# Kernel tuning notes

Measured on AMD Instinct MI355X. Metric: run time of the kernel, lower is better.

The kernel has to match this reference:

```python
import jax, jax.numpy as jnp
import numpy as np

ALPHA = 0.2  # LeakyReLU negative slope
NEG = -9e15

def _gat_head(Wh, a1, a2, adj_mask):
    # Wh: [N,O], a1/a2: [O], adj_mask: [N,N] bool
    e = jax.nn.leaky_relu(jnp.einsum('no,o->n', Wh, a1)[:, None]
                          + jnp.einsum('no,o->n', Wh, a2)[None, :], ALPHA)
    att = jax.nn.softmax(jnp.where(adj_mask, e, NEG), axis=-1)
    return att @ Wh  # [N,O]

def setup_inputs() -> dict:
    key = jax.random.key(0)
    ks = jax.random.split(key, 6)
    N, F_IN, O, H, C = 4096, 512, 64, 8, 16
    x = jax.random.normal(ks[0], (N, F_IN), jnp.float32)
    adj = jax.random.randint(ks[1], (N, N), 0, 2, jnp.int32)
    W = jax.random.normal(ks[2], (H, F_IN, O), jnp.float32) * 0.05
    a = jax.random.normal(ks[3], (H, 2 * O), jnp.float32) * 0.05
    W_out = jax.random.normal(ks[4], (H * O, C), jnp.float32) * 0.05
    a_out = jax.random.normal(ks[5], (2 * C,), jnp.float32) * 0.05
    return {'x': x, 'adj': adj, 'W': W, 'a': a, 'W_out': W_out, 'a_out': a_out}

def reference(x, adj, W, a, W_out, a_out):
    N = x.shape[0]
    H, _, O = W.shape
    C = W_out.shape[1]
    mask = adj > 0  # [N,N]
    # multi-head attention layer (vmapped over heads)
    Wh = jnp.einsum('nf,hfo->hno', x, W)  # [H,N,O]
    a1, a2 = a[:, :O], a[:, O:]
    h_heads = jax.vmap(_gat_head, in_axes=(0, 0, 0, None))(Wh, a1, a2, mask)  # [H,N,O]
    h = jax.nn.elu(h_heads)  # concat=True -> elu per head
    h = jnp.transpose(h, (1, 0, 2)).reshape(N, H * O)  # concat heads
    # output attention layer (concat=False)
    Wh_o = h @ W_out  # [N,C]
    out = _gat_head(Wh_o, a_out[:C], a_out[C:], mask)  # [N,C]
    out = jax.nn.elu(out)
    return jax.nn.log_softmax(out, axis=1)
```

## Files before the change

### kernel.cpp

```cpp
#include <hip/hip_runtime.h>


typedef __attribute__((ext_vector_type(8))) short short8;
typedef __attribute__((ext_vector_type(4))) float f32x4;
typedef unsigned long long u64;
typedef unsigned short u16;
typedef unsigned int u32;

__device__ __forceinline__ u16 f2bf_rne(float f){
  u32 u = __float_as_uint(f);
  return (u16)((u + 0x7fffu + ((u >> 16) & 1u)) >> 16);
}
__device__ __forceinline__ void async16(void* lds, const void* g){
  __builtin_amdgcn_global_load_lds((const __attribute__((address_space(1))) u32*)g,
                                   (__attribute__((address_space(3))) u32*)lds, 16, 0, 0);
}
__device__ __forceinline__ void async4(void* lds, const void* g){
  __builtin_amdgcn_global_load_lds((const __attribute__((address_space(1))) u32*)g,
                                   (__attribute__((address_space(3))) u32*)lds, 4, 0, 0);
}

__global__ __launch_bounds__(256) void k_adj_pack(const int* __restrict__ adj,
                                                  u64* __restrict__ bits){
  int lane = threadIdx.x & 63;
  int w0 = blockIdx.x * 4 + (threadIdx.x >> 6);
  #pragma unroll
  for (int k = 0; k < 16; ++k){
    int wid = w0 + k * 16384;
    int i  = wid >> 6;
    int jg = wid & 63;
    int v = adj[(size_t)i * 4096 + (jg << 6) + lane];
    u64 m = __ballot(v != 0);
    if (lane == 0) bits[(size_t)i * 64 + jg] = m;
  }
}

__global__ __launch_bounds__(256) void k_pack_in(const float* __restrict__ x,
                                                 const float* __restrict__ W,
                                                 u16* __restrict__ xA,
                                                 u16* __restrict__ wB){
  if (blockIdx.x < 1024){
    int tid = blockIdx.x * 256 + threadIdx.x;
    int n = tid & 4095;
    int fg = tid >> 12;
    const float* src = x + (size_t)n * 512 + fg * 8;
    float4 v0 = ((const float4*)src)[0];
    float4 v1 = ((const float4*)src)[1];
    u32 pk[4];
    pk[0] = f2bf_rne(v0.x) | ((u32)f2bf_rne(v0.y) << 16);
    pk[1] = f2bf_rne(v0.z) | ((u32)f2bf_rne(v0.w) << 16);
    pk[2] = f2bf_rne(v1.x) | ((u32)f2bf_rne(v1.y) << 16);
    pk[3] = f2bf_rne(v1.z) | ((u32)f2bf_rne(v1.w) << 16);
    *(uint4*)(xA + ((size_t)fg * 4096 + n) * 8) = *(uint4*)pk;
  } else {
    int tid = (blockIdx.x - 1024) * 256 + threadIdx.x;
    int o  = tid & 63;
    int fg = (tid >> 6) & 63;
    int h  = tid >> 12;
    const float* src = W + ((size_t)h * 512 + fg * 8) * 64 + o;
    u32 pk[4];
    #pragma unroll
    for (int p = 0; p < 4; ++p){
      u16 lo = f2bf_rne(src[(2 * p) * 64]);
      u16 hi = f2bf_rne(src[(2 * p + 1) * 64]);
      pk[p] = lo | ((u32)hi << 16);
    }
    *(uint4*)(wB + (size_t)h * 32768 + ((size_t)fg * 64 + o) * 8) = *(uint4*)pk;
  }
}

__global__ __launch_bounds__(256) void k_gemm1(const u16* __restrict__ xA,
                                               const u16* __restrict__ wB,
                                               const float* __restrict__ av,
                                               u16* __restrict__ whB,
                                               float* __restrict__ e11, float* __restrict__ e102,
                                               float* __restrict__ e21, float* __restrict__ e202){
  __shared__ u16 tr[4096];
  int h    = blockIdx.y;
  int nblk = blockIdx.x;
  int lane = threadIdx.x & 63;
  int wid  = threadIdx.x >> 6;
  int row16 = lane & 15, grp = lane >> 4;
  int n0 = nblk * 64;
  int n0w = n0 + wid * 16;
  const u16* wBh = wB + (size_t)h * 32768;
  f32x4 acc[4] = {};
  #pragma unroll 4
  for (int ks = 0; ks < 16; ++ks){
    int fgb = ks * 4 + grp;
    short8 af = *(const short8*)(xA + ((size_t)fgb * 4096 + n0w + row16) * 8);
    #pragma unroll
    for (int nt = 0; nt < 4; ++nt){
      short8 bf = *(const short8*)(wBh + ((size_t)fgb * 64 + nt * 16 + row16) * 8);
      acc[nt] = __builtin_amdgcn_mfma_f32_16x16x32_bf16(af, bf, acc[nt], 0, 0, 0);
    }
  }
  float a1v[4], a2v[4];
  #pragma unroll
  for (int nt = 0; nt < 4; ++nt){
    a1v[nt] = av[h * 128 + nt * 16 + row16];
    a2v[nt] = av[h * 128 + 64 + nt * 16 + row16];
  }
  #pragma unroll
  for (int r = 0; r < 4; ++r){
    float p1 = acc[0][r] * a1v[0] + acc[1][r] * a1v[1] + acc[2][r] * a1v[2] + acc[3][r] * a1v[3];
    float p2 = acc[0][r] * a2v[0] + acc[1][r] * a2v[1] + acc[2][r] * a2v[2] + acc[3][r] * a2v[3];
    #pragma unroll
    for (int d = 1; d < 16; d <<= 1){ p1 += __shfl_xor(p1, d, 64); p2 += __shfl_xor(p2, d, 64); }
    if (row16 == 0){
      int idx = h * 4096 + n0w + grp * 4 + r;
      e11[idx]  = __expf(p1); e102[idx] = __expf(0.2f * p1);
      e21[idx]  = __expf(p2); e202[idx] = __expf(0.2f * p2);
    }
  }
  #pragma unroll
  for (int nt = 0; nt < 4; ++nt)
    #pragma unroll
    for (int r = 0; r < 4; ++r){
      int jl = wid * 16 + grp * 4 + r;
      int o  = nt * 16 + row16;
      tr[((jl >> 3) * 64 + o) * 8 + (jl & 7)] = f2bf_rne(acc[nt][r]);
    }
  __syncthreads();
  u16* dst = whB + (size_t)h * 262144 + (size_t)n0 * 64;
  #pragma unroll
  for (int q = 0; q < 2; ++q)
    *(uint4*)(dst + (threadIdx.x * 2 + q) * 8) = *(const uint4*)(tr + (threadIdx.x * 2 + q) * 8);
}

__global__ __launch_bounds__(256) void k_att1(const u16* __restrict__ whB,
                                              const u64* __restrict__ adjbits,
                                              const float* __restrict__ e11, const float* __restrict__ e102,
                                              const float* __restrict__ e21, const float* __restrict__ e202,
                                              u16* __restrict__ pnum, float* __restrict__ pden){
  __shared__ u16  smB[2][4096];
  __shared__ float smT[2][2][64];
  __shared__ u32  smLut[4];
  int h     = blockIdx.y;
  int iblk  = blockIdx.x;
  int split = blockIdx.z;
  int lane = threadIdx.x & 63;
  int wid  = threadIdx.x >> 6;
  int row16 = lane & 15, grp = lane >> 4;
  if (threadIdx.x < 4)
    smLut[threadIdx.x] = ((threadIdx.x & 1) ? 0xFFFFu : 0u) | ((threadIdx.x & 2) ? 0xFFFF0000u : 0u);
  int ibase = iblk * 128 + wid * 32;
  int i0 = ibase + row16, i1 = ibase + 16 + row16;
  int hoff = h * 4096;
  float f1a  = e11[hoff + i0],  f1b  = e11[hoff + i1];
  float f02a = e102[hoff + i0], f02b = e102[hoff + i1];
  const u16* whBh = whB + (size_t)h * 262144;
  int jbeg = split * 1024;

  short8 bden;
  #pragma unroll
  for (int t = 0; t < 8; ++t) bden[t] = (row16 == 0) ? (short)0x3F80 : (short)0;

  auto stage = [&](int b, int j0){
    const char* g = (const char*)whBh + (size_t)j0 * 128 + wid * 2048 + lane * 16;
    char* l = (char*)(&smB[b][0]) + wid * 2048;
    async16(l, g);
    async16(l + 1024, g + 1024);
    if (wid == 0)      async4(&smT[b][0][0], (const char*)(e21  + hoff + j0) + lane * 4);
    else if (wid == 1) async4(&smT[b][1][0], (const char*)(e202 + hoff + j0) + lane * 4);
  };

  f32x4 acc[2][4] = {};
  f32x4 accden[2] = {};
  stage(0, jbeg);
  for (int c = 0; c < 16; ++c){
    int b = c & 1;
    u64 mrow0 = adjbits[(size_t)i0 * 64 + ((jbeg + c * 64) >> 6)];
    u64 mrow1 = adjbits[(size_t)i1 * 64 + ((jbeg + c * 64) >> 6)];
    __syncthreads();
    if (c < 15) stage(b ^ 1, jbeg + (c + 1) * 64);
    #pragma unroll
    for (int ks = 0; ks < 2; ++ks){
      int kb = ks * 32 + grp * 8;
      float4 eA = *(const float4*)(&smT[b][0][kb]);
      float4 eB = *(const float4*)(&smT[b][0][kb + 4]);
      float4 gA = *(const float4*)(&smT[b][1][kb]);
      float4 gB = *(const float4*)(&smT[b][1][kb + 4]);
      float e1v[8] = {eA.x, eA.y, eA.z, eA.w, eB.x, eB.y, eB.z, eB.w};
      float e2v[8] = {gA.x, gA.y, gA.z, gA.w, gB.x, gB.y, gB.z, gB.w};
      const u16* bbase = &smB[b][(ks * 4 + grp) * 512];
      short8 bf0 = *(const short8*)(bbase + (0 * 16 + row16) * 8);
      short8 bf1 = *(const short8*)(bbase + (1 * 16 + row16) * 8);
      short8 bf2 = *(const short8*)(bbase + (2 * 16 + row16) * 8);
      short8 bf3 = *(const short8*)(bbase + (3 * 16 + row16) * 8);
      #pragma unroll
      for (int it = 0; it < 2; ++it){
        u64 mrow = it ? mrow1 : mrow0;
        float f1 = it ? f1b : f1a;
        float f02 = it ? f02b : f02a;
        u32 mb = ((u32)(mrow >> (ks * 32)) >> (grp * 8)) & 0xffu;
        u32 pk[4];
        #pragma unroll
        for (int t2 = 0; t2 < 4; ++t2){
          float w0 = fmaxf(f1 * e1v[2 * t2],     f02 * e2v[2 * t2]);
          float w1 = fmaxf(f1 * e1v[2 * t2 + 1], f02 * e2v[2 * t2 + 1]);
          u32 p = __builtin_amdgcn_perm(__float_as_uint(w1), __float_as_uint(w0), 0x07060302u);
          pk[t2] = p & smLut[(mb >> (2 * t2)) & 3u];
        }
        short8 af = *(short8*)pk;
        acc[it][0] = __builtin_amdgcn_mfma_f32_16x16x32_bf16(af, bf0, acc[it][0], 0, 0, 0);
        acc[it][1] = __builtin_amdgcn_mfma_f32_16x16x32_bf16(af, bf1, acc[it][1], 0, 0, 0);
        acc[it][2] = __builtin_amdgcn_mfma_f32_16x16x32_bf16(af, bf2, acc[it][2], 0, 0, 0);
        acc[it][3] = __builtin_amdgcn_mfma_f32_16x16x32_bf16(af, bf3, acc[it][3], 0, 0, 0);
        accden[it] = __builtin_amdgcn_mfma_f32_16x16x32_bf16(af, bden, accden[it], 0, 0, 0);
      }
    }
  }

  #pragma unroll
  for (int it = 0; it < 2; ++it){
    #pragma unroll
    for (int r = 0; r < 4; ++r){
      int n = ibase + it * 16 + grp * 4 + r;
      if (row16 == 0)
        pden[((size_t)split * 8 + h) * 4096 + n] = accden[it][r];
      u16* dst = pnum + ((size_t)split * 4096 + n) * 512 + h * 64 + row16;
      #pragma unroll
      for (int nt = 0; nt < 4; ++nt)
        dst[nt * 16] = f2bf_rne(acc[it][nt][r]);
    }
  }
}

__global__ __launch_bounds__(256) void k_gemm2(const u16* __restrict__ pnum,
                                               const float* __restrict__ pden,
                                               const float* __restrict__ Wout,
                                               const float* __restrict__ aout,
                                               u16* __restrict__ whoB,
                                               float* __restrict__ e11o, float* __restrict__ e102o,
                                               float* __restrict__ e21o, float* __restrict__ e202o){
  __shared__ float Wl[8192];
  __shared__ float hrow[16 * 516];
  __shared__ float sden[128];
  int n0 = blockIdx.x * 16;
  for (int t = threadIdx.x; t < 8192; t += 256) Wl[t] = Wout[t];
  if (threadIdx.x < 128){
    int hh = threadIdx.x >> 4, nn = threadIdx.x & 15;
    float d = 0.f;
    #pragma unroll
    for (int s = 0; s < 4; ++s) d += pden[((size_t)s * 8 + hh) * 4096 + n0 + nn];
    sden[threadIdx.x] = d;
  }
  __syncthreads();
  {
    int nn = threadIdx.x >> 4;
    int fc = threadIdx.x & 15;
    int f0 = fc * 32;
    int hh = fc >> 1;
    float dinv = 1.f / sden[hh * 16 + nn];
    float v[32];
    #pragma unroll
    for (int k = 0; k < 32; ++k) v[k] = 0.f;
    #pragma unroll
    for (int s = 0; s < 4; ++s){
      const u16* p = pnum + ((size_t)s * 4096 + n0 + nn) * 512 + f0;
      #pragma unroll
      for (int q = 0; q < 4; ++q){
        uint4 raw = *(const uint4*)(p + q * 8);
        u32 rw[4] = {raw.x, raw.y, raw.z, raw.w};
        #pragma unroll
        for (int d2 = 0; d2 < 4; ++d2){
          v[q * 8 + d2 * 2]     += __uint_as_float(rw[d2] << 16);
          v[q * 8 + d2 * 2 + 1] += __uint_as_float(rw[d2] & 0xffff0000u);
        }
      }
    }
    #pragma unroll
    for (int k = 0; k < 32; ++k){
      float val = v[k] * dinv;
      val = val > 0.f ? val : (__expf(val) - 1.f);
      hrow[nn * 516 + f0 + k] = val;
    }
  }
  __syncthreads();
  int c  = threadIdx.x & 15;
  int rl = threadIdx.x >> 4;
  int n = n0 + rl;
  const float4* hr = (const float4*)(hrow + rl * 516);
  float acc = 0.f;
  #pragma unroll 8
  for (int f4 = 0; f4 < 128; ++f4){
    float4 hv = hr[f4];
    int f = f4 * 4;
    acc += hv.x * Wl[f * 16 + c] + hv.y * Wl[(f + 1) * 16 + c]
         + hv.z * Wl[(f + 2) * 16 + c] + hv.w * Wl[(f + 3) * 16 + c];
  }
  whoB[((size_t)(n >> 3) * 16 + c) * 8 + (n & 7)] = f2bf_rne(acc);
  float p1 = acc * aout[c], p2 = acc * aout[16 + c];
  #pragma unroll
  for (int d = 1; d < 16; d <<= 1){ p1 += __shfl_xor(p1, d, 64); p2 += __shfl_xor(p2, d, 64); }
  if (c == 0){
    e11o[n] = __expf(p1); e102o[n] = __expf(0.2f * p1);
    e21o[n] = __expf(p2); e202o[n] = __expf(0.2f * p2);
  }
}

__global__ __launch_bounds__(256) void k_att2(const u16* __restrict__ whoB,
                                              const u64* __restrict__ adjbits,
                                              const float* __restrict__ e11o, const float* __restrict__ e102o,
                                              const float* __restrict__ e21o, const float* __restrict__ e202o,
                                              float* __restrict__ pnum, float* __restrict__ pden){
  __shared__ u16  smB[2][1024];
  __shared__ float smT[2][2][64];
  __shared__ u32  smLut[4];
  int iblk  = blockIdx.x;
  int split = blockIdx.y;
  int lane = threadIdx.x & 63;
  int wid  = threadIdx.x >> 6;
  int row16 = lane & 15, grp = lane >> 4;
  if (threadIdx.x < 4)
    smLut[threadIdx.x] = ((threadIdx.x & 1) ? 0xFFFFu : 0u) | ((threadIdx.x & 2) ? 0xFFFF0000u : 0u);
  int i = iblk * 64 + wid * 16 + row16;
  float f1  = e11o[i];
  float f02 = e102o[i];
  int jbeg = split * 256;
  short8 bden;
  #pragma unroll
  for (int t = 0; t < 8; ++t) bden[t] = (row16 == 0) ? (short)0x3F80 : (short)0;

  auto stage = [&](int b, int j0){
    const char* gB = (const char*)whoB + (size_t)j0 * 32;
    if (wid == 0){
      async16((char*)&smB[b][0], gB + lane * 16);
      async16((char*)&smB[b][0] + 1024, gB + 1024 + lane * 16);
    }
    else if (wid == 1) async4(&smT[b][0][0], (const char*)(e21o  + j0) + lane * 4);
    else if (wid == 2) async4(&smT[b][1][0], (const char*)(e202o + j0) + lane * 4);
  };

  f32x4 acc = {};
  f32x4 accden = {};
  stage(0, jbeg);
  for (int c = 0; c < 4; ++c){
    int b = c & 1;
    u64 mrow = adjbits[(size_t)i * 64 + ((jbeg + c * 64) >> 6)];
    __syncthreads();
    if (c < 3) stage(b ^ 1, jbeg + (c + 1) * 64);
    #pragma unroll
    for (int ks = 0; ks < 2; ++ks){
      int kb = ks * 32 + grp * 8;
      float4 eA = *(const float4*)(&smT[b][0][kb]);
      float4 eB = *(const float4*)(&smT[b][0][kb + 4]);
      float4 gA = *(const float4*)(&smT[b][1][kb]);
      float4 gB = *(const float4*)(&smT[b][1][kb + 4]);
      float e1v[8] = {eA.x, eA.y, eA.z, eA.w, eB.x, eB.y, eB.z, eB.w};
      float e2v[8] = {gA.x, gA.y, gA.z, gA.w, gB.x, gB.y, gB.z, gB.w};
      u32 mb = ((u32)(mrow >> (ks * 32)) >> (grp * 8)) & 0xffu;
      u32 pk[4];
      #pragma unroll
      for (int t2 = 0; t2 < 4; ++t2){
        float w0 = fmaxf(f1 * e1v[2 * t2],     f02 * e2v[2 * t2]);
        float w1 = fmaxf(f1 * e1v[2 * t2 + 1], f02 * e2v[2 * t2 + 1]);
        u32 p = __builtin_amdgcn_perm(__float_as_uint(w1), __float_as_uint(w0), 0x07060302u);
        pk[t2] = p & smLut[(mb >> (2 * t2)) & 3u];
      }
      short8 af = *(short8*)pk;
      short8 bf = *(const short8*)(&smB[b][((ks * 4 + grp) * 16 + row16) * 8]);
      acc    = __builtin_amdgcn_mfma_f32_16x16x32_bf16(af, bf, acc, 0, 0, 0);
      accden = __builtin_amdgcn_mfma_f32_16x16x32_bf16(af, bden, accden, 0, 0, 0);
    }
  }
  #pragma unroll
  for (int r = 0; r < 4; ++r){
    int n = iblk * 64 + wid * 16 + grp * 4 + r;
    if (row16 == 0)
      pden[(size_t)n * 16 + split] = accden[r];
    pnum[((size_t)n * 16 + split) * 16 + row16] = acc[r];
  }
}

__global__ __launch_bounds__(256) void k_final(const float* __restrict__ pnum,
                                               const float* __restrict__ pden,
                                               float* __restrict__ out){
  int tid = blockIdx.x * 256 + threadIdx.x;
  int c = tid & 15;
  int n = tid >> 4;
  float num = 0.f, den = 0.f;
  #pragma unroll
  for (int s = 0; s < 16; ++s){
    num += pnum[((size_t)n * 16 + s) * 16 + c];
    den += pden[(size_t)n * 16 + s];
  }
  float v = num / den;
  v = v > 0.f ? v : (__expf(v) - 1.f);
  float m = v;
  #pragma unroll
  for (int d = 1; d < 16; d <<= 1) m = fmaxf(m, __shfl_xor(m, d, 64));
  float es = __expf(v - m), ss = es;
  #pragma unroll
  for (int d = 1; d < 16; d <<= 1) ss += __shfl_xor(ss, d, 64);
  out[(size_t)n * 16 + c] = v - m - __logf(ss);
}

extern "C" void kernel_launch(void* const* d_in, const int* in_sizes, int n_in,
                              void* d_out, int out_size, void* d_ws, size_t ws_size,
                              hipStream_t stream){
  (void)in_sizes; (void)n_in; (void)out_size; (void)ws_size;
  const float* x    = (const float*)d_in[0];
  const int*   adj  = (const int*)d_in[1];
  const float* W    = (const float*)d_in[2];
  const float* av   = (const float*)d_in[3];
  const float* Wout = (const float*)d_in[4];
  const float* aout = (const float*)d_in[5];
  float* out = (float*)d_out;
  char* ws = (char*)d_ws;

  u64*  adjbits = (u64*)(ws + 0x0000000);
  u16*  whB     = (u16*)(ws + 0x0200000);
  float* e11    = (float*)(ws + 0x0600000);
  float* e102   = (float*)(ws + 0x0620000);
  float* e21    = (float*)(ws + 0x0640000);
  float* e202   = (float*)(ws + 0x0660000);
  u16*  xA    = (u16*)(ws + 0x0680000);
  u16*  wB    = (u16*)(ws + 0x0A80000);
  u16*  pnum1 = (u16*)(ws + 0x0680000);
  float* pden1 = (float*)(ws + 0x1680000);
  u16*  whoB   = (u16*)(ws + 0x1700000);
  float* e11o  = (float*)(ws + 0x1720000);
  float* e102o = (float*)(ws + 0x1724000);
  float* e21o  = (float*)(ws + 0x1728000);
  float* e202o = (float*)(ws + 0x172C000);
  float* pnum2 = (float*)(ws + 0x1730000);
  float* pden2 = (float*)(ws + 0x1B30000);

  k_adj_pack<<<dim3(4096), dim3(256), 0, stream>>>(adj, adjbits);
  k_pack_in<<<dim3(1152), dim3(256), 0, stream>>>(x, W, xA, wB);
  k_gemm1<<<dim3(64, 8), dim3(256), 0, stream>>>(xA, wB, av, whB, e11, e102, e21, e202);
  k_att1<<<dim3(32, 8, 4), dim3(256), 0, stream>>>(whB, adjbits, e11, e102, e21, e202, pnum1, pden1);
  k_gemm2<<<dim3(256), dim3(256), 0, stream>>>(pnum1, pden1, Wout, aout, whoB, e11o, e102o, e21o, e202o);
  k_att2<<<dim3(64, 16), dim3(256), 0, stream>>>(whoB, adjbits, e11o, e102o, e21o, e202o, pnum2, pden2);
  k_final<<<dim3(256), dim3(256), 0, stream>>>(pnum2, pden2, out);
}
```

Baseline: 194.1 us.

## Load attention B-operands directly from global instead of LDS double-buffer staging

Both attention kernels drop the async global-to-LDS double-buffered staging of the value tiles and exp-score vectors. Each wave now reads its MFMA B fragments and score vectors straight from global memory, relying on L1/L2 caching, which removes the per-chunk block barriers and the LDS traffic. The cost is that the four waves re-fetch the same tiles redundantly through cache, with no explicit prefetch to hide load latency.

Measured after the change: 213.6 us. +10.1%, slower.

```diff
diff --git a/kernel.cpp b/kernel.cpp
--- a/kernel.cpp
+++ b/kernel.cpp
@@ -10,14 +10,6 @@
 __device__ __forceinline__ u16 f2bf_rne(float f){
   u32 u = __float_as_uint(f);
   return (u16)((u + 0x7fffu + ((u >> 16) & 1u)) >> 16);
-}
-__device__ __forceinline__ void async16(void* lds, const void* g){
-  __builtin_amdgcn_global_load_lds((const __attribute__((address_space(1))) u32*)g,
-                                   (__attribute__((address_space(3))) u32*)lds, 16, 0, 0);
-}
-__device__ __forceinline__ void async4(void* lds, const void* g){
-  __builtin_amdgcn_global_load_lds((const __attribute__((address_space(1))) u32*)g,
-                                   (__attribute__((address_space(3))) u32*)lds, 4, 0, 0);
 }
 
 __global__ __launch_bounds__(256) void k_adj_pack(const int* __restrict__ adj,
@@ -133,9 +125,7 @@
                                               const float* __restrict__ e11, const float* __restrict__ e102,
                                               const float* __restrict__ e21, const float* __restrict__ e202,
                                               u16* __restrict__ pnum, float* __restrict__ pden){
-  __shared__ u16  smB[2][4096];
-  __shared__ float smT[2][2][64];
-  __shared__ u32  smLut[4];
+  __shared__ u32 smLut[4];
   int h     = blockIdx.y;
   int iblk  = blockIdx.x;
   int split = blockIdx.z;
@@ -144,6 +134,7 @@
   int row16 = lane & 15, grp = lane >> 4;
   if (threadIdx.x < 4)
     smLut[threadIdx.x] = ((threadIdx.x & 1) ? 0xFFFFu : 0u) | ((threadIdx.x & 2) ? 0xFFFF0000u : 0u);
+  __syncthreads();
   int ibase = iblk * 128 + wid * 32;
   int i0 = ibase + row16, i1 = ibase + 16 + row16;
   int hoff = h * 4096;
@@ -156,38 +147,29 @@
   #pragma unroll
   for (int t = 0; t < 8; ++t) bden[t] = (row16 == 0) ? (short)0x3F80 : (short)0;
 
-  auto stage = [&](int b, int j0){
-    const char* g = (const char*)whBh + (size_t)j0 * 128 + wid * 2048 + lane * 16;
-    char* l = (char*)(&smB[b][0]) + wid * 2048;
-    async16(l, g);
-    async16(l + 1024, g + 1024);
-    if (wid == 0)      async4(&smT[b][0][0], (const char*)(e21  + hoff + j0) + lane * 4);
-    else if (wid == 1) async4(&smT[b][1][0], (const char*)(e202 + hoff + j0) + lane * 4);
-  };
-
   f32x4 acc[2][4] = {};
   f32x4 accden[2] = {};
-  stage(0, jbeg);
+  #pragma unroll 2
   for (int c = 0; c < 16; ++c){
-    int b = c & 1;
-    u64 mrow0 = adjbits[(size_t)i0 * 64 + ((jbeg + c * 64) >> 6)];
-    u64 mrow1 = adjbits[(size_t)i1 * 64 + ((jbeg + c * 64) >> 6)];
-    __syncthreads();
-    if (c < 15) stage(b ^ 1, jbeg + (c + 1) * 64);
+    int j0 = jbeg + c * 64;
+    u64 mrow0 = adjbits[(size_t)i0 * 64 + (j0 >> 6)];
+    u64 mrow1 = adjbits[(size_t)i1 * 64 + (j0 >> 6)];
     #pragma unroll
     for (int ks = 0; ks < 2; ++ks){
-      int kb = ks * 32 + grp * 8;
-      float4 eA = *(const float4*)(&smT[b][0][kb]);
-      float4 eB = *(const float4*)(&smT[b][0][kb + 4]);
-      float4 gA = *(const float4*)(&smT[b][1][kb]);
-      float4 gB = *(const float4*)(&smT[b][1][kb + 4]);
+      int sb = (j0 >> 3) + ks * 4 + grp;
+      const u16* bb = whBh + ((size_t)sb * 64) * 8;
+      short8 bf0 = *(const short8*)(bb + (0 * 16 + row16) * 8);
+      short8 bf1 = *(const short8*)(bb + (1 * 16 + row16) * 8);
+      short8 bf2 = *(const short8*)(bb + (2 * 16 + row16) * 8);
+      short8 bf3 = *(const short8*)(bb + (3 * 16 + row16) * 8);
+      const float* t1 = e21  + hoff + j0 + ks * 32 + grp * 8;
+      const float* t2 = e202 + hoff + j0 + ks * 32 + grp * 8;
+      float4 eA = *(const float4*)t1;
+      float4 eB = *(const float4*)(t1 + 4);
+      float4 gA = *(const float4*)t2;
+      float4 gB = *(const float4*)(t2 + 4);
       float e1v[8] = {eA.x, eA.y, eA.z, eA.w, eB.x, eB.y, eB.z, eB.w};
       float e2v[8] = {gA.x, gA.y, gA.z, gA.w, gB.x, gB.y, gB.z, gB.w};
-      const u16* bbase = &smB[b][(ks * 4 + grp) * 512];
-      short8 bf0 = *(const short8*)(bbase + (0 * 16 + row16) * 8);
-      short8 bf1 = *(const short8*)(bbase + (1 * 16 + row16) * 8);
-      short8 bf2 = *(const short8*)(bbase + (2 * 16 + row16) * 8);
-      short8 bf3 = *(const short8*)(bbase + (3 * 16 + row16) * 8);
       #pragma unroll
       for (int it = 0; it < 2; ++it){
         u64 mrow = it ? mrow1 : mrow0;
@@ -196,11 +178,11 @@
         u32 mb = ((u32)(mrow >> (ks * 32)) >> (grp * 8)) & 0xffu;
         u32 pk[4];
         #pragma unroll
-        for (int t2 = 0; t2 < 4; ++t2){
-          float w0 = fmaxf(f1 * e1v[2 * t2],     f02 * e2v[2 * t2]);
-          float w1 = fmaxf(f1 * e1v[2 * t2 + 1], f02 * e2v[2 * t2 + 1]);
+        for (int t2i = 0; t2i < 4; ++t2i){
+          float w0 = fmaxf(f1 * e1v[2 * t2i],     f02 * e2v[2 * t2i]);
+          float w1 = fmaxf(f1 * e1v[2 * t2i + 1], f02 * e2v[2 * t2i + 1]);
           u32 p = __builtin_amdgcn_perm(__float_as_uint(w1), __float_as_uint(w0), 0x07060302u);
-          pk[t2] = p & smLut[(mb >> (2 * t2)) & 3u];
+          pk[t2i] = p & smLut[(mb >> (2 * t2i)) & 3u];
         }
         short8 af = *(short8*)pk;
         acc[it][0] = __builtin_amdgcn_mfma_f32_16x16x32_bf16(af, bf0, acc[it][0], 0, 0, 0);
@@ -305,9 +287,7 @@
                                               const float* __restrict__ e11o, const float* __restrict__ e102o,
                                               const float* __restrict__ e21o, const float* __restrict__ e202o,
                                               float* __restrict__ pnum, float* __restrict__ pden){
-  __shared__ u16  smB[2][1024];
-  __shared__ float smT[2][2][64];
-  __shared__ u32  smLut[4];
+  __shared__ u32 smLut[4];
   int iblk  = blockIdx.x;
   int split = blockIdx.y;
   int lane = threadIdx.x & 63;
@@ -315,6 +295,7 @@
   int row16 = lane & 15, grp = lane >> 4;
   if (threadIdx.x < 4)
     smLut[threadIdx.x] = ((threadIdx.x & 1) ? 0xFFFFu : 0u) | ((threadIdx.x & 2) ? 0xFFFF0000u : 0u);
+  __syncthreads();
   int i = iblk * 64 + wid * 16 + row16;
   float f1  = e11o[i];
   float f02 = e102o[i];
@@ -323,44 +304,34 @@
   #pragma unroll
   for (int t = 0; t < 8; ++t) bden[t] = (row16 == 0) ? (short)0x3F80 : (short)0;
 
-  auto stage = [&](int b, int j0){
-    const char* gB = (const char*)whoB + (size_t)j0 * 32;
-    if (wid == 0){
-      async16((char*)&smB[b][0], gB + lane * 16);
-      async16((char*)&smB[b][0] + 1024, gB + 1024 + lane * 16);
-    }
-    else if (wid == 1) async4(&smT[b][0][0], (const char*)(e21o  + j0) + lane * 4);
-    else if (wid == 2) async4(&smT[b][1][0], (const char*)(e202o + j0) + lane * 4);
-  };
-
   f32x4 acc = {};
   f32x4 accden = {};
-  stage(0, jbeg);
+  #pragma unroll
   for (int c = 0; c < 4; ++c){
-    int b = c & 1;
-    u64 mrow = adjbits[(size_t)i * 64 + ((jbeg + c * 64) >> 6)];
-    __syncthreads();
-    if (c < 3) stage(b ^ 1, jbeg + (c + 1) * 64);
+    int j0 = jbeg + c * 64;
+    u64 mrow = adjbits[(size_t)i * 64 + (j0 >> 6)];
     #pragma unroll
     for (int ks = 0; ks < 2; ++ks){
-      int kb = ks * 32 + grp * 8;
-      float4 eA = *(const float4*)(&smT[b][0][kb]);
-      float4 eB = *(const float4*)(&smT[b][0][kb + 4]);
-      float4 gA = *(const float4*)(&smT[b][1][kb]);
-      float4 gB = *(const float4*)(&smT[b][1][kb + 4]);
+      int sb = (j0 >> 3) + ks * 4 + grp;
+      short8 bf = *(const short8*)(whoB + ((size_t)sb * 16 + row16) * 8);
+      const float* t1 = e21o  + j0 + ks * 32 + grp * 8;
+      const float* t2 = e202o + j0 + ks * 32 + grp * 8;
+      float4 eA = *(const float4*)t1;
+      float4 eB = *(const float4*)(t1 + 4);
+      float4 gA = *(const float4*)t2;
+      float4 gB = *(const float4*)(t2 + 4);
       float e1v[8] = {eA.x, eA.y, eA.z, eA.w, eB.x, eB.y, eB.z, eB.w};
       float e2v[8] = {gA.x, gA.y, gA.z, gA.w, gB.x, gB.y, gB.z, gB.w};
       u32 mb = ((u32)(mrow >> (ks * 32)) >> (grp * 8)) & 0xffu;
       u32 pk[4];
       #pragma unroll
-      for (int t2 = 0; t2 < 4; ++t2){
-        float w0 = fmaxf(f1 * e1v[2 * t2],     f02 * e2v[2 * t2]);
-        float w1 = fmaxf(f1 * e1v[2 * t2 + 1], f02 * e2v[2 * t2 + 1]);
+      for (int t2i = 0; t2i < 4; ++t2i){
+        float w0 = fmaxf(f1 * e1v[2 * t2i],     f02 * e2v[2 * t2i]);
+        float w1 = fmaxf(f1 * e1v[2 * t2i + 1], f02 * e2v[2 * t2i + 1]);
         u32 p = __builtin_amdgcn_perm(__float_as_uint(w1), __float_as_uint(w0), 0x07060302u);
-        pk[t2] = p & smLut[(mb >> (2 * t2)) & 3u];
+        pk[t2i] = p & smLut[(mb >> (2 * t2i)) & 3u];
       }
       short8 af = *(short8*)pk;
-      short8 bf = *(const short8*)(&smB[b][((ks * 4 + grp) * 16 + row16) * 8]);
       acc    = __builtin_amdgcn_mfma_f32_16x16x32_bf16(af, bf, acc, 0, 0, 0);
       accden = __builtin_amdgcn_mfma_f32_16x16x32_bf16(af, bden, accden, 0, 0, 0);
     }
```
